# Kernel optimization log

Hardware: AMD Instinct MI355X
Metric: run time of the kernel (lower is better)

## Reference

```python
import jax, jax.numpy as jnp
import numpy as np

D_MODEL = 1024
NHEAD = 16
D_K = D_MODEL // NHEAD


def sparsemax(z):
    # sparsemax along last axis (Martins & Astudillo 2016)
    n = z.shape[-1]
    z_sorted = jnp.flip(jnp.sort(z, axis=-1), axis=-1)          # descending
    k = jnp.arange(1, n + 1, dtype=z.dtype)
    z_cumsum = jnp.cumsum(z_sorted, axis=-1)
    support = (1.0 + k * z_sorted) > z_cumsum                    # [..., n] bool
    k_max = jnp.sum(support, axis=-1, keepdims=True)             # [..., 1] int
    tau_sum = jnp.take_along_axis(z_cumsum, k_max - 1, axis=-1)
    tau = (tau_sum - 1.0) / k_max.astype(z.dtype)
    return jnp.maximum(z - tau, 0.0)


def setup_inputs() -> dict:
    key = jax.random.key(0)
    ks = jax.random.split(key, 12)
    B, S = 2, 2048
    s = 1.0 / np.sqrt(D_MODEL)
    inp = {
        'query': jax.random.normal(ks[0], (B, S, D_MODEL), jnp.float32),
        'key':   jax.random.normal(ks[1], (B, S, D_MODEL), jnp.float32),
        'value': jax.random.normal(ks[2], (B, S, D_MODEL), jnp.float32),
        'Wq': jax.random.uniform(ks[3], (D_MODEL, D_MODEL), jnp.float32, -s, s),
        'bq': jax.random.uniform(ks[4], (D_MODEL,), jnp.float32, -s, s),
        'Wk': jax.random.uniform(ks[5], (D_MODEL, D_MODEL), jnp.float32, -s, s),
        'bk': jax.random.uniform(ks[6], (D_MODEL,), jnp.float32, -s, s),
        'Wv': jax.random.uniform(ks[7], (D_MODEL, D_MODEL), jnp.float32, -s, s),
        'bv': jax.random.uniform(ks[8], (D_MODEL,), jnp.float32, -s, s),
        'Wfc': jax.random.uniform(ks[9], (D_MODEL, D_MODEL), jnp.float32, -s, s),
        'bfc': jax.random.uniform(ks[10], (D_MODEL,), jnp.float32, -s, s),
    }
    return inp


def reference(query, key, value, Wq, bq, Wk, bk, Wv, bv, Wfc, bfc):
    B, S, _ = query.shape
    # projections (torch Linear: x @ W.T + b)
    q = (query @ Wq.T + bq).reshape(B, S, NHEAD, D_K).transpose(0, 2, 1, 3)
    k = (key   @ Wk.T + bk).reshape(B, S, NHEAD, D_K).transpose(0, 2, 1, 3)
    v = (value @ Wv.T + bv).reshape(B, S, NHEAD, D_K).transpose(0, 2, 1, 3)
    # scaled dot-product with sparsemax
    logits = jnp.einsum('bhqd,bhkd->bhqk', q, k) / np.sqrt(D_K).astype(jnp.float32)
    attention = sparsemax(logits)                                # [B,H,S,S]
    attn_out = jnp.einsum('bhqk,bhkd->bhqd', attention, v)
    attn_out = attn_out.transpose(0, 2, 1, 3).reshape(B, S, D_MODEL)
    output = attn_out @ Wfc.T + bfc                              # dropout = identity (eval)
    return output, attention
```

## Files before the change

kernel.cpp:

```cpp
#include <hip/hip_runtime.h>
#include <hip/hip_bf16.h>
#include <cstdint>

#define S_LEN  2048
#define DMODEL 1024
#define NHEAD  16
#define M_ROWS 4096

typedef __attribute__((ext_vector_type(8))) short bf16x8;
typedef __attribute__((ext_vector_type(4))) float f32x4;

__device__ __forceinline__ unsigned short f2bf(float f) {
    __hip_bfloat16 h = __float2bfloat16(f);
    return __builtin_bit_cast(unsigned short, h);
}
__device__ __forceinline__ float bf2f(unsigned short u) {
    return __builtin_bit_cast(float, (unsigned)u << 16);
}
__device__ __forceinline__ uint4 pack8(float4 a, float4 b) {
    uint4 u;
    u.x = ((unsigned)f2bf(a.y) << 16) | f2bf(a.x);
    u.y = ((unsigned)f2bf(a.w) << 16) | f2bf(a.z);
    u.z = ((unsigned)f2bf(b.y) << 16) | f2bf(b.x);
    u.w = ((unsigned)f2bf(b.w) << 16) | f2bf(b.z);
    return u;
}

__device__ __forceinline__ float wave_sum64(float v) {
    v += __shfl_xor(v, 32, 64); v += __shfl_xor(v, 16, 64);
    v += __shfl_xor(v, 8, 64);  v += __shfl_xor(v, 4, 64);
    v += __shfl_xor(v, 2, 64);  v += __shfl_xor(v, 1, 64);
    return v;
}
__device__ __forceinline__ float wave_max64(float v) {
    v = fmaxf(v, __shfl_xor(v, 32, 64)); v = fmaxf(v, __shfl_xor(v, 16, 64));
    v = fmaxf(v, __shfl_xor(v, 8, 64));  v = fmaxf(v, __shfl_xor(v, 4, 64));
    v = fmaxf(v, __shfl_xor(v, 2, 64));  v = fmaxf(v, __shfl_xor(v, 1, 64));
    return v;
}
__device__ __forceinline__ int lanes_below(unsigned long long m) {
    return __builtin_amdgcn_mbcnt_hi((unsigned)(m >> 32),
           __builtin_amdgcn_mbcnt_lo((unsigned)m, 0));
}

__global__ __launch_bounds__(256)
void qkv_gemm(const float* __restrict__ xq, const float* __restrict__ xk,
              const float* __restrict__ xv,
              const float* __restrict__ Wq, const float* __restrict__ Wk,
              const float* __restrict__ Wv,
              const float* __restrict__ bq, const float* __restrict__ bk,
              const float* __restrict__ bv,
              unsigned short* __restrict__ Q_bf, unsigned short* __restrict__ K_bf,
              unsigned short* __restrict__ V_bf) {
    const int which = blockIdx.z;
    const float* A    = (which == 0) ? xq : (which == 1) ? xk : xv;
    const float* W    = (which == 0) ? Wq : (which == 1) ? Wk : Wv;
    const float* bias = (which == 0) ? bq : (which == 1) ? bk : bv;
    unsigned short* dst = (which == 0) ? Q_bf : (which == 1) ? K_bf : V_bf;
    const float qscale = (which == 0) ? 0.125f : 1.0f;

    const int row0 = blockIdx.x * 128;
    const int col0 = blockIdx.y * 128;

    __shared__ unsigned short SMEM[10240];
    unsigned short* As = SMEM;
    unsigned short* Bs = SMEM + 5120;

    const int t = threadIdx.x;
    const int wid = t >> 6, lane = t & 63;
    const int wm = wid >> 1, wn = wid & 1;
    const int l = lane & 15, quad = lane >> 4;

    f32x4 acc[4][4];
#pragma unroll
    for (int i = 0; i < 4; ++i)
#pragma unroll
        for (int j = 0; j < 4; ++j) {
            float b_ = bias[col0 + wn * 64 + j * 16 + l];
            acc[i][j] = (f32x4){ b_, b_, b_, b_ };
        }

    for (int k0 = 0; k0 < DMODEL; k0 += 32) {
        uint4 ar[2], br[2];
#pragma unroll
        for (int i = 0; i < 2; ++i) {
            const int c = t + i * 256, r = c >> 2, q = (c & 3) * 8;
            const float* ap = A + (size_t)(row0 + r) * DMODEL + k0 + q;
            const float* wp = W + (size_t)(col0 + r) * DMODEL + k0 + q;
            float4 a0 = *(const float4*)ap, a1 = *(const float4*)(ap + 4);
            float4 w0 = *(const float4*)wp, w1 = *(const float4*)(wp + 4);
            ar[i] = pack8(a0, a1);
            br[i] = pack8(w0, w1);
        }
        __syncthreads();
#pragma unroll
        for (int i = 0; i < 2; ++i) {
            const int c = t + i * 256, r = c >> 2, q = (c & 3) * 8;
            *(uint4*)&As[r * 40 + q] = ar[i];
            *(uint4*)&Bs[r * 40 + q] = br[i];
        }
        __syncthreads();
        bf16x8 a[4], b[4];
#pragma unroll
        for (int i = 0; i < 4; ++i)
            a[i] = *(const bf16x8*)&As[(wm * 64 + i * 16 + l) * 40 + quad * 8];
#pragma unroll
        for (int j = 0; j < 4; ++j)
            b[j] = *(const bf16x8*)&Bs[(wn * 64 + j * 16 + l) * 40 + quad * 8];
#pragma unroll
        for (int i = 0; i < 4; ++i)
#pragma unroll
            for (int j = 0; j < 4; ++j)
                acc[i][j] = __builtin_amdgcn_mfma_f32_16x16x32_bf16(a[i], b[j], acc[i][j], 0, 0, 0);
    }

    __syncthreads();
    unsigned short* Cs = SMEM;
#pragma unroll 1
    for (int jh = 0; jh < 2; ++jh) {
        if (wn == jh) {
#pragma unroll
            for (int i = 0; i < 4; ++i)
#pragma unroll
                for (int j = 0; j < 4; ++j)
#pragma unroll
                    for (int r = 0; r < 4; ++r)
                        Cs[(wm * 64 + i * 16 + quad * 4 + r) * 72 + j * 16 + l] =
                            f2bf(acc[i][j][r] * qscale);
        }
        __syncthreads();
#pragma unroll
        for (int it = 0; it < 4; ++it) {
            const int idx = t + it * 256;
            const int row = idx >> 3, c8 = (idx & 7) * 8;
            *(uint4*)(dst + (size_t)(row0 + row) * DMODEL + col0 + jh * 64 + c8) =
                *(const uint4*)&Cs[row * 72 + c8];
        }
        __syncthreads();
    }
}

__global__ __launch_bounds__(512, 6)
void attn_fused(const unsigned short* __restrict__ Q_bf,
                const unsigned short* __restrict__ K_bf,
                const unsigned short* __restrict__ V_bf,
                float* __restrict__ attn,
                unsigned short* __restrict__ AO_bf) {
    const int t = threadIdx.x;
    const int w = t >> 6, lane = t & 63;
    const int l = lane & 15, quad = lane >> 4;
    const int bh = blockIdx.y, b_ = bh >> 4, h = bh & 15;
    const int r0 = blockIdx.x * 8;

    __shared__ uint2 List[8 * 512];
    float* LDSf = (float*)List;

    const unsigned short* Qp =
        Q_bf + ((size_t)(b_ * S_LEN + r0 + (l & 7))) * DMODEL + h * 64 + quad * 8;
    const bf16x8 a0 = *(const bf16x8*)Qp;
    const bf16x8 a1 = *(const bf16x8*)(Qp + 32);

    float z[32];
    float m = -__builtin_inff();
#pragma unroll
    for (int q = 0; q < 4; ++q) {
        const unsigned short* Kb =
            K_bf + ((size_t)(b_ * S_LEN + q * 512 + w * 64 + l)) * DMODEL
            + h * 64 + quad * 8;
        f32x4 acc[4];
#pragma unroll
        for (int ct = 0; ct < 4; ++ct) {
            const unsigned short* Kp = Kb + (size_t)(ct * 16) * DMODEL;
            const bf16x8 b0 = *(const bf16x8*)Kp;
            const bf16x8 b1 = *(const bf16x8*)(Kp + 32);
            f32x4 c = {};
            c = __builtin_amdgcn_mfma_f32_16x16x32_bf16(a0, b0, c, 0, 0, 0);
            c = __builtin_amdgcn_mfma_f32_16x16x32_bf16(a1, b1, c, 0, 0, 0);
            acc[ct] = c;
        }
        if (quad < 2) {
#pragma unroll
            for (int ct = 0; ct < 4; ++ct)
#pragma unroll
                for (int r = 0; r < 4; ++r)
                    LDSf[(quad * 4 + r) * 512 + w * 64 + ct * 16 + l] = acc[ct][r];
        }
        __syncthreads();
#pragma unroll
        for (int j = 0; j < 8; ++j) {
            z[q * 8 + j] = LDSf[w * 512 + j * 64 + lane];
            m = fmaxf(m, z[q * 8 + j]);
        }
        __syncthreads();
    }

    m = wave_max64(m);
    const float thr = m - 1.0f;

    uint2* list = List + w * 512;
    int cnt = 0;
#pragma unroll
    for (int jj = 0; jj < 32; ++jj) {
        const float zv = z[jj];
        const unsigned long long mk = __ballot(zv > thr);
        if (zv > thr) {
            const int pos = cnt + lanes_below(mk);
            if (pos < 512)
                list[pos] = (uint2){ (unsigned)((jj >> 3) * 512 + (jj & 7) * 64 + lane),
                                     __builtin_bit_cast(unsigned, zv) };
        }
        cnt += __popcll(mk);
    }
    __threadfence_block();

    float tau = thr;
    if (cnt <= 256) {
        const float NEG = -__builtin_inff();
        const float zc0 = (lane < cnt)
            ? __builtin_bit_cast(float, list[lane].y) : NEG;
        const float zc1 = (64 + lane < cnt)
            ? __builtin_bit_cast(float, list[64 + lane].y) : NEG;
        const float zc2 = (128 + lane < cnt)
            ? __builtin_bit_cast(float, list[128 + lane].y) : NEG;
        const float zc3 = (192 + lane < cnt)
            ? __builtin_bit_cast(float, list[192 + lane].y) : NEG;
#pragma unroll 1
        for (int it = 0; it < 12; ++it) {
            float ss = 0.0f, kk = 0.0f;
            if (zc0 > tau) { ss += zc0; kk += 1.0f; }
            if (zc1 > tau) { ss += zc1; kk += 1.0f; }
            if (zc2 > tau) { ss += zc2; kk += 1.0f; }
            if (zc3 > tau) { ss += zc3; kk += 1.0f; }
            ss = wave_sum64(ss); kk = wave_sum64(kk);
            const float tn = (ss - 1.0f) / kk;
            if (tn == tau) break;
            tau = tn;
        }
    } else {
#pragma unroll 1
        for (int it = 0; it < 8; ++it) {
            float ss = 0.0f, kk = 0.0f;
#pragma unroll
            for (int j = 0; j < 32; ++j)
                if (z[j] > tau) { ss += z[j]; kk += 1.0f; }
            ss = wave_sum64(ss); kk = wave_sum64(kk);
            const float tn = (ss - 1.0f) / kk;
            if (tn == tau) break;
            tau = tn;
        }
        cnt = 0;
#pragma unroll
        for (int jj = 0; jj < 32; ++jj) {
            const float zv = z[jj];
            const unsigned long long mk = __ballot(zv > tau);
            if (zv > tau) {
                const int pos = cnt + lanes_below(mk);
                if (pos < 512)
                    list[pos] = (uint2){ (unsigned)((jj >> 3) * 512 + (jj & 7) * 64 + lane),
                                         __builtin_bit_cast(unsigned, zv) };
            }
            cnt += __popcll(mk);
        }
        __threadfence_block();
    }
    if (cnt > 504) cnt = 504;

    float* ap = attn + (size_t)bh * S_LEN * S_LEN + (size_t)(r0 + w) * S_LEN;
#pragma unroll
    for (int jj = 0; jj < 32; ++jj) {
        const float pv = fmaxf(z[jj] - tau, 0.0f);
        __builtin_nontemporal_store(pv, ap + (jj >> 3) * 512 + (jj & 7) * 64 + lane);
    }

    if (lane < 8)
        list[cnt + lane] = (uint2){ 0u, 0xff800000u };
    __threadfence_block();

    const unsigned short* Vh = V_bf + ((size_t)b_ * S_LEN) * DMODEL + h * 64;
    const int sub = lane >> 3, dbase = (lane & 7) * 8;
    float acc8[8] = {};
    const int gmax = (cnt + 7) >> 3;
#pragma unroll 2
    for (int g = 0; g < gmax; ++g) {
        const uint2 e = list[g * 8 + sub];
        const float p = fmaxf(__builtin_bit_cast(float, e.y) - tau, 0.0f);
        const uint4 vv = *(const uint4*)(Vh + ((size_t)e.x) * DMODEL + dbase);
        acc8[0] += p * bf2f((unsigned short)(vv.x & 0xffff));
        acc8[1] += p * bf2f((unsigned short)(vv.x >> 16));
        acc8[2] += p * bf2f((unsigned short)(vv.y & 0xffff));
        acc8[3] += p * bf2f((unsigned short)(vv.y >> 16));
        acc8[4] += p * bf2f((unsigned short)(vv.z & 0xffff));
        acc8[5] += p * bf2f((unsigned short)(vv.z >> 16));
        acc8[6] += p * bf2f((unsigned short)(vv.w & 0xffff));
        acc8[7] += p * bf2f((unsigned short)(vv.w >> 16));
    }
#pragma unroll
    for (int d = 0; d < 8; ++d) {
        acc8[d] += __shfl_xor(acc8[d], 8, 64);
        acc8[d] += __shfl_xor(acc8[d], 16, 64);
        acc8[d] += __shfl_xor(acc8[d], 32, 64);
    }
    if (lane < 8) {
        union { unsigned short u[8]; uint4 v; } o;
#pragma unroll
        for (int d = 0; d < 8; ++d) o.u[d] = f2bf(acc8[d]);
        *(uint4*)(AO_bf + ((size_t)(b_ * S_LEN + r0 + w)) * DMODEL
                  + h * 64 + lane * 8) = o.v;
    }
}

__global__ __launch_bounds__(256)
void fc_gemm(const unsigned short* __restrict__ AO_bf,
             const float* __restrict__ Wfc,
             const float* __restrict__ bfc, float* __restrict__ out) {
    const int row0 = blockIdx.x * 128;
    const int col0 = blockIdx.y * 128;

    __shared__ unsigned short As[128 * 40];
    __shared__ unsigned short Bs[128 * 40];

    const int t = threadIdx.x;
    const int wid = t >> 6, lane = t & 63;
    const int wm = wid >> 1, wn = wid & 1;
    const int l = lane & 15, quad = lane >> 4;

    f32x4 acc[4][4];
#pragma unroll
    for (int i = 0; i < 4; ++i)
#pragma unroll
        for (int j = 0; j < 4; ++j) {
            float b_ = bfc[col0 + wn * 64 + j * 16 + l];
            acc[i][j] = (f32x4){ b_, b_, b_, b_ };
        }

    for (int k0 = 0; k0 < DMODEL; k0 += 32) {
        uint4 ar[2], br[2];
#pragma unroll
        for (int i = 0; i < 2; ++i) {
            const int c = t + i * 256, r = c >> 2, q = (c & 3) * 8;
            ar[i] = *(const uint4*)(AO_bf + (size_t)(row0 + r) * DMODEL + k0 + q);
            const float* wp = Wfc + (size_t)(col0 + r) * DMODEL + k0 + q;
            float4 w0 = *(const float4*)wp, w1 = *(const float4*)(wp + 4);
            br[i] = pack8(w0, w1);
        }
        __syncthreads();
#pragma unroll
        for (int i = 0; i < 2; ++i) {
            const int c = t + i * 256, r = c >> 2, q = (c & 3) * 8;
            *(uint4*)&As[r * 40 + q] = ar[i];
            *(uint4*)&Bs[r * 40 + q] = br[i];
        }
        __syncthreads();
        bf16x8 a[4], b[4];
#pragma unroll
        for (int i = 0; i < 4; ++i)
            a[i] = *(const bf16x8*)&As[(wm * 64 + i * 16 + l) * 40 + quad * 8];
#pragma unroll
        for (int j = 0; j < 4; ++j)
            b[j] = *(const bf16x8*)&Bs[(wn * 64 + j * 16 + l) * 40 + quad * 8];
#pragma unroll
        for (int i = 0; i < 4; ++i)
#pragma unroll
            for (int j = 0; j < 4; ++j)
                acc[i][j] = __builtin_amdgcn_mfma_f32_16x16x32_bf16(a[i], b[j], acc[i][j], 0, 0, 0);
    }

#pragma unroll
    for (int i = 0; i < 4; ++i)
#pragma unroll
        for (int r = 0; r < 4; ++r) {
            const int m = row0 + wm * 64 + i * 16 + quad * 4 + r;
#pragma unroll
            for (int j = 0; j < 4; ++j) {
                const int n = col0 + wn * 64 + j * 16 + l;
                out[(size_t)m * DMODEL + n] = acc[i][j][r];
            }
        }
}

extern "C" void kernel_launch(void* const* d_in, const int* in_sizes, int n_in,
                              void* d_out, int out_size, void* d_ws, size_t ws_size,
                              hipStream_t stream) {
    const float* q   = (const float*)d_in[0];
    const float* k   = (const float*)d_in[1];
    const float* v   = (const float*)d_in[2];
    const float* Wq  = (const float*)d_in[3];
    const float* bq  = (const float*)d_in[4];
    const float* Wk  = (const float*)d_in[5];
    const float* bk  = (const float*)d_in[6];
    const float* Wv  = (const float*)d_in[7];
    const float* bv  = (const float*)d_in[8];
    const float* Wfc = (const float*)d_in[9];
    const float* bfc = (const float*)d_in[10];

    float* out  = (float*)d_out;
    float* attn = out + (size_t)M_ROWS * DMODEL;

    char* ws = (char*)d_ws;
    unsigned short* Q_bf  = (unsigned short*)ws;
    unsigned short* K_bf  = (unsigned short*)(ws + (8u << 20));
    unsigned short* V_bf  = (unsigned short*)(ws + (16u << 20));
    unsigned short* AO_bf = (unsigned short*)(ws + (24u << 20));

    qkv_gemm<<<dim3(32, 8, 3), 256, 0, stream>>>(q, k, v, Wq, Wk, Wv,
                                                  bq, bk, bv, Q_bf, K_bf, V_bf);
    attn_fused<<<dim3(S_LEN / 8, 32), 512, 0, stream>>>(Q_bf, K_bf, V_bf, attn, AO_bf);
    fc_gemm<<<dim3(32, 8), 256, 0, stream>>>(AO_bf, Wfc, bfc, out);
}
```

Before: 914.1 us.

## Pre-convert QKV inputs to bf16 and compact sparsemax support list with probabilities

Adds a separate conversion kernel that turns the fp32 activations and weights into bf16 once, staged in the attention output buffer as scratch, so the QKV GEMM reads half the bytes and skips repeated in-loop packing. The sparsemax path now rewrites the list to hold only the final support entries with precomputed probabilities (z - tau), removing the per-element subtraction and the padding entries in the PV loop. The PV gather loop is unrolled to issue four V row loads per iteration, raising memory-level parallelism. The trade-offs are an extra kernel launch plus a full pass over the inputs, some __threadfence_block calls being dropped, and a lower list cap of 480.

```diff
diff --git a/kernel.cpp b/kernel.cpp
--- a/kernel.cpp
+++ b/kernel.cpp
@@ -44,18 +44,41 @@
 }
 
 __global__ __launch_bounds__(256)
-void qkv_gemm(const float* __restrict__ xq, const float* __restrict__ xk,
+void cvt_bf16(const float* __restrict__ xq, const float* __restrict__ xk,
               const float* __restrict__ xv,
               const float* __restrict__ Wq, const float* __restrict__ Wk,
               const float* __restrict__ Wv,
+              unsigned short* __restrict__ oXq, unsigned short* __restrict__ oXk,
+              unsigned short* __restrict__ oXv,
+              unsigned short* __restrict__ oWq, unsigned short* __restrict__ oWk,
+              unsigned short* __restrict__ oWv) {
+    const int y = blockIdx.y;
+    const float* src = (y == 0) ? xq : (y == 1) ? xk : (y == 2) ? xv
+                     : (y == 3) ? Wq : (y == 4) ? Wk : Wv;
+    unsigned short* dst = (y == 0) ? oXq : (y == 1) ? oXk : (y == 2) ? oXv
+                        : (y == 3) ? oWq : (y == 4) ? oWk : oWv;
+    const int n = (y < 3) ? (M_ROWS * DMODEL) : (DMODEL * DMODEL);
+    const int stride = gridDim.x * blockDim.x * 8;
+    for (int i = (blockIdx.x * blockDim.x + threadIdx.x) * 8; i < n; i += stride) {
+        float4 a = *(const float4*)(src + i);
+        float4 b = *(const float4*)(src + i + 4);
+        *(uint4*)(dst + i) = pack8(a, b);
+    }
+}
+
+__global__ __launch_bounds__(256)
+void qkv_gemm(const unsigned short* __restrict__ Xq, const unsigned short* __restrict__ Xk,
+              const unsigned short* __restrict__ Xv,
+              const unsigned short* __restrict__ Wqb, const unsigned short* __restrict__ Wkb,
+              const unsigned short* __restrict__ Wvb,
               const float* __restrict__ bq, const float* __restrict__ bk,
               const float* __restrict__ bv,
               unsigned short* __restrict__ Q_bf, unsigned short* __restrict__ K_bf,
               unsigned short* __restrict__ V_bf) {
     const int which = blockIdx.z;
-    const float* A    = (which == 0) ? xq : (which == 1) ? xk : xv;
-    const float* W    = (which == 0) ? Wq : (which == 1) ? Wk : Wv;
-    const float* bias = (which == 0) ? bq : (which == 1) ? bk : bv;
+    const unsigned short* A = (which == 0) ? Xq : (which == 1) ? Xk : Xv;
+    const unsigned short* W = (which == 0) ? Wqb : (which == 1) ? Wkb : Wvb;
+    const float* bias  = (which == 0) ? bq : (which == 1) ? bk : bv;
     unsigned short* dst = (which == 0) ? Q_bf : (which == 1) ? K_bf : V_bf;
     const float qscale = (which == 0) ? 0.125f : 1.0f;
 
@@ -85,12 +108,8 @@
 #pragma unroll
         for (int i = 0; i < 2; ++i) {
             const int c = t + i * 256, r = c >> 2, q = (c & 3) * 8;
-            const float* ap = A + (size_t)(row0 + r) * DMODEL + k0 + q;
-            const float* wp = W + (size_t)(col0 + r) * DMODEL + k0 + q;
-            float4 a0 = *(const float4*)ap, a1 = *(const float4*)(ap + 4);
-            float4 w0 = *(const float4*)wp, w1 = *(const float4*)(wp + 4);
-            ar[i] = pack8(a0, a1);
-            br[i] = pack8(w0, w1);
+            ar[i] = *(const uint4*)(A + (size_t)(row0 + r) * DMODEL + k0 + q);
+            br[i] = *(const uint4*)(W + (size_t)(col0 + r) * DMODEL + k0 + q);
         }
         __syncthreads();
 #pragma unroll
@@ -211,19 +230,19 @@
         }
         cnt += __popcll(mk);
     }
-    __threadfence_block();
 
     float tau = thr;
+    int scnt = 0;
     if (cnt <= 256) {
         const float NEG = -__builtin_inff();
-        const float zc0 = (lane < cnt)
-            ? __builtin_bit_cast(float, list[lane].y) : NEG;
-        const float zc1 = (64 + lane < cnt)
-            ? __builtin_bit_cast(float, list[64 + lane].y) : NEG;
-        const float zc2 = (128 + lane < cnt)
-            ? __builtin_bit_cast(float, list[128 + lane].y) : NEG;
-        const float zc3 = (192 + lane < cnt)
-            ? __builtin_bit_cast(float, list[192 + lane].y) : NEG;
+        const uint2 E0 = list[lane];
+        const uint2 E1 = list[64 + lane];
+        const uint2 E2 = list[128 + lane];
+        const uint2 E3 = list[192 + lane];
+        const float zc0 = (lane < cnt)       ? __builtin_bit_cast(float, E0.y) : NEG;
+        const float zc1 = (64 + lane < cnt)  ? __builtin_bit_cast(float, E1.y) : NEG;
+        const float zc2 = (128 + lane < cnt) ? __builtin_bit_cast(float, E2.y) : NEG;
+        const float zc3 = (192 + lane < cnt) ? __builtin_bit_cast(float, E3.y) : NEG;
 #pragma unroll 1
         for (int it = 0; it < 12; ++it) {
             float ss = 0.0f, kk = 0.0f;
@@ -236,6 +255,23 @@
             if (tn == tau) break;
             tau = tn;
         }
+        unsigned long long mk;
+        mk = __ballot(zc0 > tau);
+        if (zc0 > tau) list[scnt + lanes_below(mk)] =
+            (uint2){ E0.x, __builtin_bit_cast(unsigned, zc0 - tau) };
+        scnt += __popcll(mk);
+        mk = __ballot(zc1 > tau);
+        if (zc1 > tau) list[scnt + lanes_below(mk)] =
+            (uint2){ E1.x, __builtin_bit_cast(unsigned, zc1 - tau) };
+        scnt += __popcll(mk);
+        mk = __ballot(zc2 > tau);
+        if (zc2 > tau) list[scnt + lanes_below(mk)] =
+            (uint2){ E2.x, __builtin_bit_cast(unsigned, zc2 - tau) };
+        scnt += __popcll(mk);
+        mk = __ballot(zc3 > tau);
+        if (zc3 > tau) list[scnt + lanes_below(mk)] =
+            (uint2){ E3.x, __builtin_bit_cast(unsigned, zc3 - tau) };
+        scnt += __popcll(mk);
     } else {
 #pragma unroll 1
         for (int it = 0; it < 8; ++it) {
@@ -248,22 +284,20 @@
             if (tn == tau) break;
             tau = tn;
         }
-        cnt = 0;
 #pragma unroll
         for (int jj = 0; jj < 32; ++jj) {
             const float zv = z[jj];
             const unsigned long long mk = __ballot(zv > tau);
             if (zv > tau) {
-                const int pos = cnt + lanes_below(mk);
-                if (pos < 512)
+                const int pos = scnt + lanes_below(mk);
+                if (pos < 480)
                     list[pos] = (uint2){ (unsigned)((jj >> 3) * 512 + (jj & 7) * 64 + lane),
-                                         __builtin_bit_cast(unsigned, zv) };
+                                         __builtin_bit_cast(unsigned, zv - tau) };
             }
-            cnt += __popcll(mk);
-        }
-        __threadfence_block();
-    }
-    if (cnt > 504) cnt = 504;
+            scnt += __popcll(mk);
+        }
+        if (scnt > 480) scnt = 480;
+    }
 
     float* ap = attn + (size_t)bh * S_LEN * S_LEN + (size_t)(r0 + w) * S_LEN;
 #pragma unroll
@@ -272,27 +306,60 @@
         __builtin_nontemporal_store(pv, ap + (jj >> 3) * 512 + (jj & 7) * 64 + lane);
     }
 
-    if (lane < 8)
-        list[cnt + lane] = (uint2){ 0u, 0xff800000u };
-    __threadfence_block();
+    if (lane < 32)
+        list[scnt + lane] = (uint2){ 0u, 0u };
 
     const unsigned short* Vh = V_bf + ((size_t)b_ * S_LEN) * DMODEL + h * 64;
     const int sub = lane >> 3, dbase = (lane & 7) * 8;
     float acc8[8] = {};
-    const int gmax = (cnt + 7) >> 3;
-#pragma unroll 2
-    for (int g = 0; g < gmax; ++g) {
-        const uint2 e = list[g * 8 + sub];
-        const float p = fmaxf(__builtin_bit_cast(float, e.y) - tau, 0.0f);
-        const uint4 vv = *(const uint4*)(Vh + ((size_t)e.x) * DMODEL + dbase);
-        acc8[0] += p * bf2f((unsigned short)(vv.x & 0xffff));
-        acc8[1] += p * bf2f((unsigned short)(vv.x >> 16));
-        acc8[2] += p * bf2f((unsigned short)(vv.y & 0xffff));
-        acc8[3] += p * bf2f((unsigned short)(vv.y >> 16));
-        acc8[4] += p * bf2f((unsigned short)(vv.z & 0xffff));
-        acc8[5] += p * bf2f((unsigned short)(vv.z >> 16));
-        acc8[6] += p * bf2f((unsigned short)(vv.w & 0xffff));
-        acc8[7] += p * bf2f((unsigned short)(vv.w >> 16));
+    const int gmax4 = (scnt + 31) >> 5;
+#pragma unroll 1
+    for (int g = 0; g < gmax4; ++g) {
+        const int b0 = g * 32 + sub;
+        const uint2 e0 = list[b0];
+        const uint2 e1 = list[b0 + 8];
+        const uint2 e2 = list[b0 + 16];
+        const uint2 e3 = list[b0 + 24];
+        const uint4 v0 = *(const uint4*)(Vh + (size_t)e0.x * DMODEL + dbase);
+        const uint4 v1 = *(const uint4*)(Vh + (size_t)e1.x * DMODEL + dbase);
+        const uint4 v2 = *(const uint4*)(Vh + (size_t)e2.x * DMODEL + dbase);
+        const uint4 v3 = *(const uint4*)(Vh + (size_t)e3.x * DMODEL + dbase);
+        const float p0 = __builtin_bit_cast(float, e0.y);
+        const float p1 = __builtin_bit_cast(float, e1.y);
+        const float p2 = __builtin_bit_cast(float, e2.y);
+        const float p3 = __builtin_bit_cast(float, e3.y);
+        acc8[0] += p0 * bf2f((unsigned short)(v0.x & 0xffff));
+        acc8[1] += p0 * bf2f((unsigned short)(v0.x >> 16));
+        acc8[2] += p0 * bf2f((unsigned short)(v0.y & 0xffff));
+        acc8[3] += p0 * bf2f((unsigned short)(v0.y >> 16));
+        acc8[4] += p0 * bf2f((unsigned short)(v0.z & 0xffff));
+        acc8[5] += p0 * bf2f((unsigned short)(v0.z >> 16));
+        acc8[6] += p0 * bf2f((unsigned short)(v0.w & 0xffff));
+        acc8[7] += p0 * bf2f((unsigned short)(v0.w >> 16));
+        acc8[0] += p1 * bf2f((unsigned short)(v1.x & 0xffff));
+        acc8[1] += p1 * bf2f((unsigned short)(v1.x >> 16));
+        acc8[2] += p1 * bf2f((unsigned short)(v1.y & 0xffff));
+        acc8[3] += p1 * bf2f((unsigned short)(v1.y >> 16));
+        acc8[4] += p1 * bf2f((unsigned short)(v1.z & 0xffff));
+        acc8[5] += p1 * bf2f((unsigned short)(v1.z >> 16));
+        acc8[6] += p1 * bf2f((unsigned short)(v1.w & 0xffff));
+        acc8[7] += p1 * bf2f((unsigned short)(v1.w >> 16));
+        acc8[0] += p2 * bf2f((unsigned short)(v2.x & 0xffff));
+        acc8[1] += p2 * bf2f((unsigned short)(v2.x >> 16));
+        acc8[2] += p2 * bf2f((unsigned short)(v2.y & 0xffff));
+        acc8[3] += p2 * bf2f((unsigned short)(v2.y >> 16));
+        acc8[4] += p2 * bf2f((unsigned short)(v2.z & 0xffff));
+        acc8[5] += p2 * bf2f((unsigned short)(v2.z >> 16));
+        acc8[6] += p2 * bf2f((unsigned short)(v2.w & 0xffff));
+        acc8[7] += p2 * bf2f((unsigned short)(v2.w >> 16));
+        acc8[0] += p3 * bf2f((unsigned short)(v3.x & 0xffff));
+        acc8[1] += p3 * bf2f((unsigned short)(v3.x >> 16));
+        acc8[2] += p3 * bf2f((unsigned short)(v3.y & 0xffff));
+        acc8[3] += p3 * bf2f((unsigned short)(v3.y >> 16));
+        acc8[4] += p3 * bf2f((unsigned short)(v3.z & 0xffff));
+        acc8[5] += p3 * bf2f((unsigned short)(v3.z >> 16));
+        acc8[6] += p3 * bf2f((unsigned short)(v3.w & 0xffff));
+        acc8[7] += p3 * bf2f((unsigned short)(v3.w >> 16));
     }
 #pragma unroll
     for (int d = 0; d < 8; ++d) {
@@ -396,13 +463,23 @@
     float* out  = (float*)d_out;
     float* attn = out + (size_t)M_ROWS * DMODEL;
 
+    char* sc = (char*)attn;
+    unsigned short* Xq  = (unsigned short*)sc;
+    unsigned short* Xk  = (unsigned short*)(sc + (8u << 20));
+    unsigned short* Xv  = (unsigned short*)(sc + (16u << 20));
+    unsigned short* Wqb = (unsigned short*)(sc + (24u << 20));
+    unsigned short* Wkb = (unsigned short*)(sc + (26u << 20));
+    unsigned short* Wvb = (unsigned short*)(sc + (28u << 20));
+
     char* ws = (char*)d_ws;
     unsigned short* Q_bf  = (unsigned short*)ws;
     unsigned short* K_bf  = (unsigned short*)(ws + (8u << 20));
     unsigned short* V_bf  = (unsigned short*)(ws + (16u << 20));
     unsigned short* AO_bf = (unsigned short*)(ws + (24u << 20));
 
-    qkv_gemm<<<dim3(32, 8, 3), 256, 0, stream>>>(q, k, v, Wq, Wk, Wv,
+    cvt_bf16<<<dim3(512, 6), 256, 0, stream>>>(q, k, v, Wq, Wk, Wv,
+                                               Xq, Xk, Xv, Wqb, Wkb, Wvb);
+    qkv_gemm<<<dim3(32, 8, 3), 256, 0, stream>>>(Xq, Xk, Xv, Wqb, Wkb, Wvb,
                                                   bq, bk, bv, Q_bf, K_bf, V_bf);
     attn_fused<<<dim3(S_LEN / 8, 32), 512, 0, stream>>>(Q_bf, K_bf, V_bf, attn, AO_bf);
     fc_gemm<<<dim3(32, 8), 256, 0, stream>>>(AO_bf, Wfc, bfc, out);
```

Result: slower. 982.0 us (+7.4%).
